# Kernel optimization log

Hardware: AMD Instinct MI355X
Metric: run time of the kernel (lower is better)

## Reference

```python
import jax, jax.numpy as jnp
import numpy as np

# Sparse grid constants (closed over; coords live on this grid)
B, H, W = 2, 640, 640
N = 409600
CIN, CH, COUT = 64, 64, 64
K = 3
PAD = (K - 1) // 2


def setup_inputs() -> dict:
    key = jax.random.key(0)
    ks = jax.random.split(key, 6)
    # unique active coordinates via permutation of the dense grid
    lin = jax.random.permutation(ks[0], B * H * W)[:N]
    b = lin // (H * W)
    rem = lin % (H * W)
    coords = jnp.stack([b, rem // W, rem % W], axis=1).astype(jnp.int32)  # [N,3]
    features = jax.random.normal(ks[1], (N, CIN), jnp.float32)
    w1 = jax.random.normal(ks[2], (K, K, CIN, CH), jnp.float32) * (1.0 / np.sqrt(K * K * CIN))
    b1 = jnp.zeros((CH,), jnp.float32)
    w2 = jax.random.normal(ks[3], (K, K, CH, COUT), jnp.float32) * (1.0 / np.sqrt(K * K * CH))
    b2 = jnp.zeros((COUT,), jnp.float32)
    wd = jax.random.normal(ks[4], (CIN, COUT), jnp.float32) * (1.0 / np.sqrt(CIN))
    return {"features": features, "coords": coords, "w1": w1, "b1": b1,
            "w2": w2, "b2": b2, "wd": wd}


def _build_grid(coords):
    # dense hash: grid[b,y,x] = row index into features, -1 if inactive
    grid = jnp.full((B, H, W), -1, dtype=jnp.int32)
    return grid.at[coords[:, 0], coords[:, 1], coords[:, 2]].set(
        jnp.arange(N, dtype=jnp.int32))


def _subm_conv(feat, coords, grid, w, bias):
    # Submanifold conv: out only at active sites; gather-matmul-accumulate per offset.
    cb, cy, cx = coords[:, 0], coords[:, 1], coords[:, 2]
    out = jnp.zeros((N, w.shape[-1]), feat.dtype)
    for ky in range(K):              # small fixed kernel loop (rulebook offsets)
        for kx in range(K):
            dy, dx = ky - PAD, kx - PAD
            ny, nx = cy + dy, cx + dx
            inb = (ny >= 0) & (ny < H) & (nx >= 0) & (nx < W)
            nidx = grid[cb, jnp.clip(ny, 0, H - 1), jnp.clip(nx, 0, W - 1)]
            valid = inb & (nidx >= 0)
            g = feat[jnp.where(valid, nidx, 0)]          # [N, Cin] gather
            g = jnp.where(valid[:, None], g, 0.0)
            out = out + g @ w[ky, kx]                    # per-offset GEMM
    if bias is not None:
        out = out + bias
    return out


def reference(features, coords, w1, b1, w2, b2, wd):
    grid = _build_grid(coords)
    out = jax.nn.relu(_subm_conv(features, coords, grid, w1, b1))
    out = jax.nn.relu(_subm_conv(out, coords, grid, w2, b2))
    residual = features @ wd                  # 1x1 subm conv, no bias
    out = jax.nn.relu(out + residual)         # sparse_add: identical index sets
    return out
```

## Files before the change

kernel.cpp:

```cpp
#include <hip/hip_runtime.h>
#include <hip/hip_bf16.h>
#include <stdint.h>

#define NP 409600
#define HG 640
#define WG 640
#define HW (HG*WG)

typedef __bf16 bf16x8 __attribute__((ext_vector_type(8)));
typedef float f32x4 __attribute__((ext_vector_type(4)));


__global__ void scatter_kernel(const int* __restrict__ coords, int* __restrict__ grid) {
    int i = blockIdx.x * 256 + threadIdx.x;
    int b = coords[3*i], y = coords[3*i+1], x = coords[3*i+2];
    grid[b*HW + y*WG + x] = i;
}

__global__ void nbr_kernel(const int* __restrict__ coords, const int* __restrict__ grid,
                           int* __restrict__ nbr) {
    int i = blockIdx.x * 256 + threadIdx.x;
    int b = coords[3*i], y = coords[3*i+1], x = coords[3*i+2];
    int baseg = b*HW;
    #pragma unroll
    for (int t = 0; t < 9; ++t) {
        int ny = y + t/3 - 1, nx = x + t%3 - 1;
        int g = -1;
        if (ny >= 0 && ny < HG && nx >= 0 && nx < WG)
            g = grid[baseg + ny*WG + nx];
        nbr[t*NP + i] = g;
    }
}

__global__ void cast_feat_kernel(const float* __restrict__ f, __hip_bfloat16* __restrict__ fb) {
    long i = (long)(blockIdx.x * 256 + threadIdx.x) * 8;
    float4 a = *(const float4*)(f + i);
    float4 b = *(const float4*)(f + i + 4);
    union { uint4 q; __hip_bfloat16 h[8]; } u;
    u.h[0] = __float2bfloat16(a.x); u.h[1] = __float2bfloat16(a.y);
    u.h[2] = __float2bfloat16(a.z); u.h[3] = __float2bfloat16(a.w);
    u.h[4] = __float2bfloat16(b.x); u.h[5] = __float2bfloat16(b.y);
    u.h[6] = __float2bfloat16(b.z); u.h[7] = __float2bfloat16(b.w);
    *(uint4*)(fb + i) = u.q;
}

__global__ void cast_w_kernel(const float* __restrict__ w1, const float* __restrict__ w2,
                              const float* __restrict__ wd,
                              __hip_bfloat16* __restrict__ wc1, __hip_bfloat16* __restrict__ wc2) {
    int i = blockIdx.x * 256 + threadIdx.x;
    if (i < 9*4096) {
        int t = i >> 12, r = i & 4095, n = r >> 6, k = r & 63;
        wc1[i] = __float2bfloat16(w1[(t << 12) + (k << 6) + n]);
    }
    int j = i - 9*4096;
    if (j >= 0 && j < 10*4096) {
        int t = j >> 12, r = j & 4095, n = r >> 6, k = r & 63;
        float v = (t < 9) ? w2[(t << 12) + (k << 6) + n] : wd[(k << 6) + n];
        wc2[j] = __float2bfloat16(v);
    }
}


#define LDA 72
#define LDB 72

template<int NTAP, bool FINAL>
__launch_bounds__(256)
__global__ void conv_kernel(const __hip_bfloat16* __restrict__ src,
                            const __hip_bfloat16* __restrict__ idsrc,
                            const int* __restrict__ nbr,
                            const __hip_bfloat16* __restrict__ wT,
                            const float* __restrict__ bias,
                            __hip_bfloat16* __restrict__ out_bf,
                            float* __restrict__ out_f) {
    __shared__ __align__(16) __hip_bfloat16 As[128 * LDA];
    __shared__ __align__(16) __hip_bfloat16 Bs[64 * LDB];

    const int tid  = threadIdx.x;
    const int base = blockIdx.x * 128;
    const int wave = tid >> 6, lane = tid & 63;
    const int srow = tid >> 1, shalf = tid & 1;

    f32x4 acc[2][4];
    f32x4 accR[2][4];
    #pragma unroll
    for (int i = 0; i < 2; ++i)
        #pragma unroll
        for (int j = 0; j < 4; ++j) {
            acc[i][j]  = (f32x4){0.f, 0.f, 0.f, 0.f};
            accR[i][j] = (f32x4){0.f, 0.f, 0.f, 0.f};
        }

    for (int t = 0; t < NTAP; ++t) {
        if (t) __syncthreads();

        int g;
        const __hip_bfloat16* sp;
        if (FINAL && t == NTAP - 1) { g = base + srow; sp = idsrc; }
        else                        { g = nbr[t*NP + base + srow]; sp = src; }
        uint4 v0, v1, v2, v3;
        if (g >= 0) {
            const uint4* p = (const uint4*)(sp + (long)g*64 + shalf*32);
            v0 = p[0]; v1 = p[1]; v2 = p[2]; v3 = p[3];
        } else {
            v0 = v1 = v2 = v3 = make_uint4(0u, 0u, 0u, 0u);
        }
        uint4* dst = (uint4*)(As + srow*LDA + shalf*32);
        dst[0] = v0; dst[1] = v1; dst[2] = v2; dst[3] = v3;

        const uint4* wp = (const uint4*)(wT + t*4096);
        #pragma unroll
        for (int j = 0; j < 2; ++j) {
            int e = tid + j*256;
            int l = e * 8;
            int n = l >> 6, k = l & 63;
            *(uint4*)(Bs + n*LDB + k) = wp[e];
        }
        __syncthreads();

        auto do_mfma = [&](f32x4 (&ac)[2][4]) {
            #pragma unroll
            for (int ks = 0; ks < 2; ++ks) {
                int kb = ks*32 + (lane >> 4)*8;
                bf16x8 a0 = *(const bf16x8*)(As + (wave*32      + (lane & 15))*LDA + kb);
                bf16x8 a1 = *(const bf16x8*)(As + (wave*32 + 16 + (lane & 15))*LDA + kb);
                bf16x8 b0 = *(const bf16x8*)(Bs + ( 0 + (lane & 15))*LDB + kb);
                bf16x8 b1 = *(const bf16x8*)(Bs + (16 + (lane & 15))*LDB + kb);
                bf16x8 b2 = *(const bf16x8*)(Bs + (32 + (lane & 15))*LDB + kb);
                bf16x8 b3 = *(const bf16x8*)(Bs + (48 + (lane & 15))*LDB + kb);
                ac[0][0] = __builtin_amdgcn_mfma_f32_16x16x32_bf16(a0, b0, ac[0][0], 0, 0, 0);
                ac[0][1] = __builtin_amdgcn_mfma_f32_16x16x32_bf16(a0, b1, ac[0][1], 0, 0, 0);
                ac[0][2] = __builtin_amdgcn_mfma_f32_16x16x32_bf16(a0, b2, ac[0][2], 0, 0, 0);
                ac[0][3] = __builtin_amdgcn_mfma_f32_16x16x32_bf16(a0, b3, ac[0][3], 0, 0, 0);
                ac[1][0] = __builtin_amdgcn_mfma_f32_16x16x32_bf16(a1, b0, ac[1][0], 0, 0, 0);
                ac[1][1] = __builtin_amdgcn_mfma_f32_16x16x32_bf16(a1, b1, ac[1][1], 0, 0, 0);
                ac[1][2] = __builtin_amdgcn_mfma_f32_16x16x32_bf16(a1, b2, ac[1][2], 0, 0, 0);
                ac[1][3] = __builtin_amdgcn_mfma_f32_16x16x32_bf16(a1, b3, ac[1][3], 0, 0, 0);
            }
        };
        if (FINAL && t == NTAP - 1) do_mfma(accR);
        else                        do_mfma(acc);
    }

    const int col = lane & 15, quad = lane >> 4;
    #pragma unroll
    for (int cb = 0; cb < 4; ++cb) {
        float bv = bias[cb*16 + col];
        #pragma unroll
        for (int mb = 0; mb < 2; ++mb) {
            #pragma unroll
            for (int r = 0; r < 4; ++r) {
                float v = acc[mb][cb][r] + bv;
                v = v > 0.f ? v : 0.f;
                long row = base + wave*32 + mb*16 + quad*4 + r;
                int  c   = cb*16 + col;
                if (FINAL) {
                    v += accR[mb][cb][r];
                    v = v > 0.f ? v : 0.f;
                    out_f[row*64 + c] = v;
                } else {
                    out_bf[row*64 + c] = __float2bfloat16(v);
                }
            }
        }
    }
}


extern "C" void kernel_launch(void* const* d_in, const int* in_sizes, int n_in,
                              void* d_out, int out_size, void* d_ws, size_t ws_size,
                              hipStream_t stream) {
    const float* features = (const float*)d_in[0];
    const int*   coords   = (const int*)d_in[1];
    const float* w1 = (const float*)d_in[2];
    const float* b1 = (const float*)d_in[3];
    const float* w2 = (const float*)d_in[4];
    const float* b2 = (const float*)d_in[5];
    const float* wd = (const float*)d_in[6];
    float* out = (float*)d_out;

    char* ws = (char*)d_ws;
    int*            grid = (int*)ws;
    int*            nbr  = (int*)(ws + 3276800);
    __hip_bfloat16* fb   = (__hip_bfloat16*)(ws + 18022400);
    __hip_bfloat16* y1   = (__hip_bfloat16*)(ws + 70451200);
    __hip_bfloat16* wc1  = (__hip_bfloat16*)(ws + 122880000);
    __hip_bfloat16* wc2  = (__hip_bfloat16*)(ws + 122953728);

    hipMemsetAsync(grid, 0xFF, (size_t)HW * 2 * sizeof(int), stream);

    scatter_kernel  <<<1600,  256, 0, stream>>>(coords, grid);
    cast_feat_kernel<<<12800, 256, 0, stream>>>(features, fb);
    cast_w_kernel   <<<304,   256, 0, stream>>>(w1, w2, wd, wc1, wc2);
    nbr_kernel      <<<1600,  256, 0, stream>>>(coords, grid, nbr);

    conv_kernel<9,  false><<<3200, 256, 0, stream>>>(fb, fb, nbr, wc1, b1, y1, nullptr);
    conv_kernel<10, true ><<<3200, 256, 0, stream>>>(y1, fb, nbr, wc2, b2, nullptr, out);
}
```

Baseline: 345.0 us.

## Compute neighbor indices inside conv kernel and prefetch next tap's gathers

```diff
diff --git a/kernel.cpp b/kernel.cpp
--- a/kernel.cpp
+++ b/kernel.cpp
@@ -11,25 +11,12 @@
 typedef float f32x4 __attribute__((ext_vector_type(4)));
 
 
-__global__ void scatter_kernel(const int* __restrict__ coords, int* __restrict__ grid) {
+__global__ void scatter_kernel(const int* __restrict__ coords, int* __restrict__ sgrid,
+                               int* __restrict__ pc) {
     int i = blockIdx.x * 256 + threadIdx.x;
     int b = coords[3*i], y = coords[3*i+1], x = coords[3*i+2];
-    grid[b*HW + y*WG + x] = i;
-}
-
-__global__ void nbr_kernel(const int* __restrict__ coords, const int* __restrict__ grid,
-                           int* __restrict__ nbr) {
-    int i = blockIdx.x * 256 + threadIdx.x;
-    int b = coords[3*i], y = coords[3*i+1], x = coords[3*i+2];
-    int baseg = b*HW;
-    #pragma unroll
-    for (int t = 0; t < 9; ++t) {
-        int ny = y + t/3 - 1, nx = x + t%3 - 1;
-        int g = -1;
-        if (ny >= 0 && ny < HG && nx >= 0 && nx < WG)
-            g = grid[baseg + ny*WG + nx];
-        nbr[t*NP + i] = g;
-    }
+    sgrid[b*HW + y*WG + x] = i;
+    pc[i] = (b << 20) | (y << 10) | x;
 }
 
 __global__ void cast_feat_kernel(const float* __restrict__ f, __hip_bfloat16* __restrict__ fb) {
@@ -68,7 +55,8 @@
 __launch_bounds__(256)
 __global__ void conv_kernel(const __hip_bfloat16* __restrict__ src,
                             const __hip_bfloat16* __restrict__ idsrc,
-                            const int* __restrict__ nbr,
+                            const int* __restrict__ pc,
+                            const int* __restrict__ sgrid,
                             const __hip_bfloat16* __restrict__ wT,
                             const float* __restrict__ bias,
                             __hip_bfloat16* __restrict__ out_bf,
@@ -81,6 +69,20 @@
     const int wave = tid >> 6, lane = tid & 63;
     const int srow = tid >> 1, shalf = tid & 1;
 
+    int g[NTAP];
+    {
+        int p = pc[base + srow];
+        int x = p & 1023, y = (p >> 10) & 1023, b = p >> 20;
+        int cell = b*HW + y*WG + x;
+        #pragma unroll
+        for (int t = 0; t < 9; ++t) {
+            int dy = t/3 - 1, dx = t%3 - 1;
+            int ny = y + dy, nx = x + dx;
+            g[t] = (ny >= 0 && ny < HG && nx >= 0 && nx < WG) ? sgrid[cell + dy*WG + dx] : -1;
+        }
+        if (FINAL) g[NTAP-1] = base + srow;
+    }
+
     f32x4 acc[2][4];
     f32x4 accR[2][4];
     #pragma unroll
@@ -91,66 +93,71 @@
             accR[i][j] = (f32x4){0.f, 0.f, 0.f, 0.f};
         }
 
+    uint4* adst = (uint4*)(As + srow*LDA + shalf*32);
+    const int e0 = tid, e1 = tid + 256;
+    const int n0 = (e0*8) >> 6, k0 = (e0*8) & 63;
+    const int n1 = (e1*8) >> 6, k1 = (e1*8) & 63;
+
+    uint4 av[4], bv[2];
+    bool vld;
+
+    auto prefetch = [&](int t) {
+        int gg = g[t];
+        const __hip_bfloat16* sp = (FINAL && t == NTAP-1) ? idsrc : src;
+        vld = gg >= 0;
+        const uint4* p = (const uint4*)(sp + (long)(gg < 0 ? 0 : gg)*64 + shalf*32);
+        av[0] = p[0]; av[1] = p[1]; av[2] = p[2]; av[3] = p[3];
+        const uint4* wp = (const uint4*)(wT + t*4096);
+        bv[0] = wp[e0]; bv[1] = wp[e1];
+    };
+
+    prefetch(0);
+
+    #pragma unroll
     for (int t = 0; t < NTAP; ++t) {
         if (t) __syncthreads();
 
-        int g;
-        const __hip_bfloat16* sp;
-        if (FINAL && t == NTAP - 1) { g = base + srow; sp = idsrc; }
-        else                        { g = nbr[t*NP + base + srow]; sp = src; }
-        uint4 v0, v1, v2, v3;
-        if (g >= 0) {
-            const uint4* p = (const uint4*)(sp + (long)g*64 + shalf*32);
-            v0 = p[0]; v1 = p[1]; v2 = p[2]; v3 = p[3];
-        } else {
-            v0 = v1 = v2 = v3 = make_uint4(0u, 0u, 0u, 0u);
-        }
-        uint4* dst = (uint4*)(As + srow*LDA + shalf*32);
-        dst[0] = v0; dst[1] = v1; dst[2] = v2; dst[3] = v3;
-
-        const uint4* wp = (const uint4*)(wT + t*4096);
-        #pragma unroll
-        for (int j = 0; j < 2; ++j) {
-            int e = tid + j*256;
-            int l = e * 8;
-            int n = l >> 6, k = l & 63;
-            *(uint4*)(Bs + n*LDB + k) = wp[e];
-        }
+        const uint4 z = make_uint4(0u,0u,0u,0u);
+        adst[0] = vld ? av[0] : z;
+        adst[1] = vld ? av[1] : z;
+        adst[2] = vld ? av[2] : z;
+        adst[3] = vld ? av[3] : z;
+        *(uint4*)(Bs + n0*LDB + k0) = bv[0];
+        *(uint4*)(Bs + n1*LDB + k1) = bv[1];
         __syncthreads();
 
-        auto do_mfma = [&](f32x4 (&ac)[2][4]) {
-            #pragma unroll
-            for (int ks = 0; ks < 2; ++ks) {
-                int kb = ks*32 + (lane >> 4)*8;
-                bf16x8 a0 = *(const bf16x8*)(As + (wave*32      + (lane & 15))*LDA + kb);
-                bf16x8 a1 = *(const bf16x8*)(As + (wave*32 + 16 + (lane & 15))*LDA + kb);
-                bf16x8 b0 = *(const bf16x8*)(Bs + ( 0 + (lane & 15))*LDB + kb);
-                bf16x8 b1 = *(const bf16x8*)(Bs + (16 + (lane & 15))*LDB + kb);
-                bf16x8 b2 = *(const bf16x8*)(Bs + (32 + (lane & 15))*LDB + kb);
-                bf16x8 b3 = *(const bf16x8*)(Bs + (48 + (lane & 15))*LDB + kb);
-                ac[0][0] = __builtin_amdgcn_mfma_f32_16x16x32_bf16(a0, b0, ac[0][0], 0, 0, 0);
-                ac[0][1] = __builtin_amdgcn_mfma_f32_16x16x32_bf16(a0, b1, ac[0][1], 0, 0, 0);
-                ac[0][2] = __builtin_amdgcn_mfma_f32_16x16x32_bf16(a0, b2, ac[0][2], 0, 0, 0);
-                ac[0][3] = __builtin_amdgcn_mfma_f32_16x16x32_bf16(a0, b3, ac[0][3], 0, 0, 0);
-                ac[1][0] = __builtin_amdgcn_mfma_f32_16x16x32_bf16(a1, b0, ac[1][0], 0, 0, 0);
-                ac[1][1] = __builtin_amdgcn_mfma_f32_16x16x32_bf16(a1, b1, ac[1][1], 0, 0, 0);
-                ac[1][2] = __builtin_amdgcn_mfma_f32_16x16x32_bf16(a1, b2, ac[1][2], 0, 0, 0);
-                ac[1][3] = __builtin_amdgcn_mfma_f32_16x16x32_bf16(a1, b3, ac[1][3], 0, 0, 0);
-            }
-        };
-        if (FINAL && t == NTAP - 1) do_mfma(accR);
-        else                        do_mfma(acc);
+        if (t + 1 < NTAP) prefetch(t + 1);
+
+        f32x4 (&ac)[2][4] = (FINAL && t == NTAP-1) ? accR : acc;
+        #pragma unroll
+        for (int ks = 0; ks < 2; ++ks) {
+            int kb = ks*32 + (lane >> 4)*8;
+            bf16x8 a0 = *(const bf16x8*)(As + (wave*32      + (lane & 15))*LDA + kb);
+            bf16x8 a1 = *(const bf16x8*)(As + (wave*32 + 16 + (lane & 15))*LDA + kb);
+            bf16x8 b0 = *(const bf16x8*)(Bs + ( 0 + (lane & 15))*LDB + kb);
+            bf16x8 b1 = *(const bf16x8*)(Bs + (16 + (lane & 15))*LDB + kb);
+            bf16x8 b2 = *(const bf16x8*)(Bs + (32 + (lane & 15))*LDB + kb);
+            bf16x8 b3 = *(const bf16x8*)(Bs + (48 + (lane & 15))*LDB + kb);
+            ac[0][0] = __builtin_amdgcn_mfma_f32_16x16x32_bf16(a0, b0, ac[0][0], 0, 0, 0);
+            ac[0][1] = __builtin_amdgcn_mfma_f32_16x16x32_bf16(a0, b1, ac[0][1], 0, 0, 0);
+            ac[0][2] = __builtin_amdgcn_mfma_f32_16x16x32_bf16(a0, b2, ac[0][2], 0, 0, 0);
+            ac[0][3] = __builtin_amdgcn_mfma_f32_16x16x32_bf16(a0, b3, ac[0][3], 0, 0, 0);
+            ac[1][0] = __builtin_amdgcn_mfma_f32_16x16x32_bf16(a1, b0, ac[1][0], 0, 0, 0);
+            ac[1][1] = __builtin_amdgcn_mfma_f32_16x16x32_bf16(a1, b1, ac[1][1], 0, 0, 0);
+            ac[1][2] = __builtin_amdgcn_mfma_f32_16x16x32_bf16(a1, b2, ac[1][2], 0, 0, 0);
+            ac[1][3] = __builtin_amdgcn_mfma_f32_16x16x32_bf16(a1, b3, ac[1][3], 0, 0, 0);
+        }
     }
 
     const int col = lane & 15, quad = lane >> 4;
     #pragma unroll
     for (int cb = 0; cb < 4; ++cb) {
-        float bv = bias[cb*16 + col];
+        float bv2 = bias[cb*16 + col];
         #pragma unroll
         for (int mb = 0; mb < 2; ++mb) {
             #pragma unroll
             for (int r = 0; r < 4; ++r) {
-                float v = acc[mb][cb][r] + bv;
+                float v = acc[mb][cb][r] + bv2;
                 v = v > 0.f ? v : 0.f;
                 long row = base + wave*32 + mb*16 + quad*4 + r;
                 int  c   = cb*16 + col;
@@ -180,20 +187,19 @@
     float* out = (float*)d_out;
 
     char* ws = (char*)d_ws;
-    int*            grid = (int*)ws;
-    int*            nbr  = (int*)(ws + 3276800);
-    __hip_bfloat16* fb   = (__hip_bfloat16*)(ws + 18022400);
-    __hip_bfloat16* y1   = (__hip_bfloat16*)(ws + 70451200);
-    __hip_bfloat16* wc1  = (__hip_bfloat16*)(ws + 122880000);
-    __hip_bfloat16* wc2  = (__hip_bfloat16*)(ws + 122953728);
-
-    hipMemsetAsync(grid, 0xFF, (size_t)HW * 2 * sizeof(int), stream);
-
-    scatter_kernel  <<<1600,  256, 0, stream>>>(coords, grid);
+    int*            sgrid = (int*)ws;
+    int*            pc    = (int*)(ws + 3276800);
+    __hip_bfloat16* fb    = (__hip_bfloat16*)(ws + 4915200);
+    __hip_bfloat16* y1    = (__hip_bfloat16*)(ws + 57344000);
+    __hip_bfloat16* wc1   = (__hip_bfloat16*)(ws + 109772800);
+    __hip_bfloat16* wc2   = (__hip_bfloat16*)(ws + 109846528);
+
+    hipMemsetAsync(sgrid, 0xFF, (size_t)HW * 2 * sizeof(int), stream);
+
+    scatter_kernel  <<<1600,  256, 0, stream>>>(coords, sgrid, pc);
     cast_feat_kernel<<<12800, 256, 0, stream>>>(features, fb);
     cast_w_kernel   <<<304,   256, 0, stream>>>(w1, w2, wd, wc1, wc2);
-    nbr_kernel      <<<1600,  256, 0, stream>>>(coords, grid, nbr);
-
-    conv_kernel<9,  false><<<3200, 256, 0, stream>>>(fb, fb, nbr, wc1, b1, y1, nullptr);
-    conv_kernel<10, true ><<<3200, 256, 0, stream>>>(y1, fb, nbr, wc2, b2, nullptr, out);
-}
+
+    conv_kernel<9,  false><<<3200, 256, 0, stream>>>(fb, fb, pc, sgrid, wc1, b1, y1, nullptr);
+    conv_kernel<10, true ><<<3200, 256, 0, stream>>>(y1, fb, pc, sgrid, wc2, b2, nullptr, out);
+}
```

After: 722.3 us. 109% more time.
